# Kernel optimization log

Measured on AMD Instinct MI355X. Metric: run time of the kernel, lower is better.

## Reference

```python
import jax, jax.numpy as jnp
import numpy as np

H = 12          # num_attention_heads
D = 64          # attention_head_size
HID = H * D     # hidden_size = 768
M = 1024        # max_position_embeddings


def setup_inputs() -> dict:
    key = jax.random.key(0)
    ks = jax.random.split(key, 9)
    B, S = 4, 1024
    s = 0.02
    return {
        "hidden_states": jax.random.normal(ks[0], (B, S, HID), jnp.float32),
        "attention_mask": jnp.zeros((B, 1, 1, S), jnp.float32),
        "Wq": jax.random.normal(ks[1], (HID, HID), jnp.float32) * s,
        "bq": jnp.zeros((HID,), jnp.float32),
        "Wk": jax.random.normal(ks[2], (HID, HID), jnp.float32) * s,
        "bk": jnp.zeros((HID,), jnp.float32),
        "Wv": jax.random.normal(ks[3], (HID, HID), jnp.float32) * s,
        "bv": jnp.zeros((HID,), jnp.float32),
        "dist_emb": jax.random.normal(ks[4], (2 * M - 1, D), jnp.float32) * s,
    }


def reference(hidden_states, attention_mask, Wq, bq, Wk, bk, Wv, bv, dist_emb):
    B, S, _ = hidden_states.shape

    def heads(x):  # [B,S,HID] -> [B,H,S,D]
        return x.reshape(B, S, H, D).transpose(0, 2, 1, 3)

    q = heads(hidden_states @ Wq + bq)
    k = heads(hidden_states @ Wk + bk)
    v = heads(hidden_states @ Wv + bv)

    # raw dot-product scores [B,H,S,S]
    scores = jnp.einsum('bhld,bhrd->bhlr', q, k)

    # relative_key_query positional bias
    pos = jnp.arange(S)
    distance = pos[:, None] - pos[None, :] + (M - 1)   # [S,S] in [0, 2M-2]
    pe = dist_emb[distance]                            # [S,S,D]
    scores = scores + jnp.einsum('bhld,lrd->bhlr', q, pe) \
                    + jnp.einsum('bhrd,lrd->bhlr', k, pe)

    scores = scores / jnp.sqrt(jnp.asarray(D, scores.dtype)) + attention_mask
    probs = jax.nn.softmax(scores, axis=-1)            # dropout is identity in eval

    ctx = jnp.einsum('bhlr,bhrd->bhld', probs, v)      # [B,H,S,D]
    ctx = ctx.transpose(0, 2, 1, 3).reshape(B, S, HID)
    return ctx, probs
```

## Files before the change

### kernel.cpp

```cpp
#include <hip/hip_runtime.h>
#include <hip/hip_bf16.h>

#define DEVFN __device__ __forceinline__

typedef __bf16 bf16x8 __attribute__((ext_vector_type(8)));
typedef float f32x4 __attribute__((ext_vector_type(4)));
typedef unsigned short ushort8 __attribute__((ext_vector_type(8)));
typedef unsigned short us4 __attribute__((ext_vector_type(4)));

namespace {

constexpr int S = 1024;
constexpr int HID = 768;
constexpr int NH = 12;
constexpr int HD = 64;

DEVFN unsigned short f2bf(float f) {
  union { float f; unsigned u; } v; v.f = f;
  unsigned r = v.u + 0x7FFF + ((v.u >> 16) & 1);
  return (unsigned short)(r >> 16);
}

DEVFN float bf2f(unsigned short u) {
  union { unsigned u; float f; } v; v.u = ((unsigned)u) << 16; return v.f;
}

DEVFN f32x4 zero4() { return f32x4{0.f, 0.f, 0.f, 0.f}; }

DEVFN f32x4 mfma_bf16(bf16x8 a, bf16x8 b, f32x4 c) {
  return __builtin_amdgcn_mfma_f32_16x16x32_bf16(a, b, c, 0, 0, 0);
}

DEVFN void gload16(void* lds_base, const void* gsrc) {
  __builtin_amdgcn_global_load_lds(
      (const __attribute__((address_space(1))) void*)gsrc,
      (__attribute__((address_space(3))) void*)lds_base, 16, 0, 0);
}

DEVFN bf16x8 frag_ld(const char* tile, int row, int ch) {
  int chs = ch ^ (row & 7);
  return *(const bf16x8*)(tile + row * 128 + chs * 16);
}

__global__ void k0_cvt_x(const float* __restrict__ x, unsigned short* __restrict__ xb) {
  size_t i = (size_t)(blockIdx.x * 256 + threadIdx.x) * 8;
  float4 a = *(const float4*)(x + i);
  float4 c = *(const float4*)(x + i + 4);
  ushort8 o;
  o[0] = f2bf(a.x); o[1] = f2bf(a.y); o[2] = f2bf(a.z); o[3] = f2bf(a.w);
  o[4] = f2bf(c.x); o[5] = f2bf(c.y); o[6] = f2bf(c.z); o[7] = f2bf(c.w);
  *(ushort8*)(xb + i) = o;
}

__global__ void k0_cvt_pe(const float* __restrict__ de, unsigned short* __restrict__ peb) {
  size_t i = (size_t)(blockIdx.x * 256 + threadIdx.x) * 8;
  int row = (int)(i >> 6);
  ushort8 o;
  if (row < 2047) {
    float4 a = *(const float4*)(de + i);
    float4 c = *(const float4*)(de + i + 4);
    o[0] = f2bf(a.x); o[1] = f2bf(a.y); o[2] = f2bf(a.z); o[3] = f2bf(a.w);
    o[4] = f2bf(c.x); o[5] = f2bf(c.y); o[6] = f2bf(c.z); o[7] = f2bf(c.w);
  } else {
    o = ushort8{0, 0, 0, 0, 0, 0, 0, 0};
  }
  *(ushort8*)(peb + i) = o;
}

__global__ __launch_bounds__(256) void k0_wt(const float* __restrict__ Wq,
                                             const float* __restrict__ Wk,
                                             const float* __restrict__ Wv,
                                             unsigned short* __restrict__ wt) {
  __shared__ float t[64][65];
  int bidx = blockIdx.x;
  int sec = bidx / 144, rem = bidx % 144;
  int ktb = rem / 12, ntb = rem % 12;
  const float* W = (sec == 0) ? Wq : ((sec == 1) ? Wk : Wv);
  int k0 = ktb * 64, n0 = ntb * 64;
  int tid = threadIdx.x;
  #pragma unroll
  for (int p = 0; p < 4; ++p) {
    int id = p * 256 + tid;
    int row = id >> 4, ch = id & 15;
    float4 v = *(const float4*)(W + (size_t)(k0 + row) * 768 + n0 + ch * 4);
    t[row][ch * 4 + 0] = v.x; t[row][ch * 4 + 1] = v.y;
    t[row][ch * 4 + 2] = v.z; t[row][ch * 4 + 3] = v.w;
  }
  __syncthreads();
  #pragma unroll
  for (int p = 0; p < 2; ++p) {
    int id = p * 256 + tid;
    int nrow = id >> 3, c8 = id & 7;
    ushort8 o;
    #pragma unroll
    for (int i = 0; i < 8; ++i) o[i] = f2bf(t[c8 * 8 + i][nrow]);
    *(ushort8*)(wt + (size_t)(sec * 768 + n0 + nrow) * 768 + k0 + c8 * 8) = o;
  }
}

__global__ __launch_bounds__(256) void k1_qkv(
    const unsigned short* __restrict__ xb, const unsigned short* __restrict__ wt,
    const float* __restrict__ bq, const float* __restrict__ bk, const float* __restrict__ bv,
    unsigned short* __restrict__ q_ws, unsigned short* __restrict__ k_ws,
    unsigned short* __restrict__ vt_ws) {
  __shared__ char ldsA[8192], ldsB[8192];
  const int tid = threadIdx.x, lane = tid & 63, wv = tid >> 6;
  const int row16 = lane & 15, cgrp = lane >> 4;
  const int ntb = blockIdx.x % 36, mtb = blockIdx.x / 36;
  const int sec = ntb / 12;
  const int n0 = ntb * 64;
  const int m0 = mtb * 64;

  f32x4 acc[4] = {zero4(), zero4(), zero4(), zero4()};

  for (int k0 = 0; k0 < 768; k0 += 64) {
    #pragma unroll
    for (int c = 0; c < 2; ++c) {
      int cc = (wv * 2 + c) * 64 + lane;
      int row = cc >> 3, ch = cc & 7, chs = ch ^ (row & 7);
      gload16(ldsA + (wv * 2 + c) * 1024, xb + (size_t)(m0 + row) * 768 + k0 + chs * 8);
      gload16(ldsB + (wv * 2 + c) * 1024, wt + (size_t)(n0 + row) * 768 + k0 + chs * 8);
    }
    __syncthreads();
    if (sec < 2) {
      bf16x8 af[2];
      #pragma unroll
      for (int k2 = 0; k2 < 2; ++k2) af[k2] = frag_ld(ldsA, wv * 16 + row16, k2 * 4 + cgrp);
      #pragma unroll
      for (int nt = 0; nt < 4; ++nt)
        #pragma unroll
        for (int k2 = 0; k2 < 2; ++k2) {
          bf16x8 bf = frag_ld(ldsB, nt * 16 + row16, k2 * 4 + cgrp);
          acc[nt] = mfma_bf16(af[k2], bf, acc[nt]);
        }
    } else {
      bf16x8 af[2];
      #pragma unroll
      for (int k2 = 0; k2 < 2; ++k2) af[k2] = frag_ld(ldsB, wv * 16 + row16, k2 * 4 + cgrp);
      #pragma unroll
      for (int mt = 0; mt < 4; ++mt)
        #pragma unroll
        for (int k2 = 0; k2 < 2; ++k2) {
          bf16x8 bx = frag_ld(ldsA, mt * 16 + row16, k2 * 4 + cgrp);
          acc[mt] = mfma_bf16(af[k2], bx, acc[mt]);
        }
    }
    __syncthreads();
  }

  if (sec < 2) {
    unsigned short* dst = (sec == 0) ? q_ws : k_ws;
    const float* bias = (sec == 0) ? bq : bk;
    int nl0 = (ntb % 12) * 64;
    #pragma unroll
    for (int nt = 0; nt < 4; ++nt) {
      int nn = nl0 + nt * 16 + row16;
      float bb = bias[nn];
      int hh = nn >> 6, dd = nn & 63;
      #pragma unroll
      for (int j = 0; j < 4; ++j) {
        int m = m0 + wv * 16 + cgrp * 4 + j;
        int b_ = m >> 10, s_ = m & 1023;
        dst[(size_t)((b_ * 12 + hh) * 1024 + s_) * 64 + dd] = f2bf(acc[nt][j] + bb);
      }
    }
  } else {
    int nl0 = (ntb % 12) * 64;
    #pragma unroll
    for (int j = 0; j < 4; ++j) {
      int nn = nl0 + wv * 16 + cgrp * 4 + j;
      float bb = bv[nn];
      int hh = nn >> 6, dd = nn & 63;
      #pragma unroll
      for (int mt = 0; mt < 4; ++mt) {
        int m = m0 + mt * 16 + row16;
        int b_ = m >> 10, s_ = m & 1023;
        vt_ws[(size_t)((b_ * 12 + hh) * 64 + dd) * 1024 + s_] = f2bf(acc[mt][j] + bb);
      }
    }
  }
}

__global__ __launch_bounds__(256) void k2_score(
    const unsigned short* __restrict__ q_ws, const unsigned short* __restrict__ k_ws,
    const unsigned short* __restrict__ peb, const float* __restrict__ mask,
    unsigned short* __restrict__ p_out, float* __restrict__ rsum_part) {
  __shared__ __align__(16) char kpe_lds[24576];
  __shared__ unsigned short p_sh[64 * 64];
  __shared__ float rsum_sh[2][64];

  char* k_lds = kpe_lds;
  char* pe_lds = kpe_lds + 8192;

  const int tid = threadIdx.x, lane = tid & 63, wv = tid >> 6;
  const int wl = wv >> 1, wr = wv & 1;
  const int row16 = lane & 15, cgrp = lane >> 4;

  const int bid = blockIdx.x;
  const int swz = (bid & 7) * 1536 + (bid >> 3);
  const int rt = swz & 15, lt = (swz >> 4) & 15, bh = swz >> 8;
  const int b = bh / NH;
  const int l0 = lt * 64, r0 = rt * 64;

  const unsigned short* qh = q_ws + (size_t)bh * S * HD;
  const unsigned short* khp = k_ws + (size_t)bh * S * HD;
  const float* maskb = mask + b * S;

  #pragma unroll
  for (int c = 0; c < 2; ++c) {
    int cc = (wv * 2 + c) * 64 + lane;
    int row = cc >> 3, ch = cc & 7, chs = ch ^ (row & 7);
    gload16(k_lds + (wv * 2 + c) * 1024, khp + (size_t)(r0 + row) * HD + chs * 8);
  }
  {
    int m0 = l0 - r0 + 960;
    #pragma unroll
    for (int c = 0; c < 4; ++c) {
      int cc = (wv * 4 + c) * 64 + lane;
      int row = cc >> 3, ch = cc & 7, chs = ch ^ (row & 7);
      gload16(pe_lds + (wv * 4 + c) * 1024, peb + (size_t)(m0 + row) * HD + chs * 8);
    }
  }

  bf16x8 qf[2][2];
  #pragma unroll
  for (int ltl = 0; ltl < 2; ++ltl)
    #pragma unroll
    for (int k2 = 0; k2 < 2; ++k2)
      qf[ltl][k2] = *(const bf16x8*)(qh + (size_t)(l0 + wl * 32 + ltl * 16 + row16) * HD +
                                     k2 * 32 + cgrp * 8);
  __syncthreads();

  bf16x8 kf[2][2], pef[4][2];
  #pragma unroll
  for (int rtl = 0; rtl < 2; ++rtl)
    #pragma unroll
    for (int k2 = 0; k2 < 2; ++k2)
      kf[rtl][k2] = frag_ld(k_lds, wr * 32 + rtl * 16 + row16, k2 * 4 + cgrp);
  const int qb = (wl - wr) * 32 + 32;
  #pragma unroll
  for (int jt = 0; jt < 4; ++jt)
    #pragma unroll
    for (int k2 = 0; k2 < 2; ++k2)
      pef[jt][k2] = frag_ld(pe_lds, qb + jt * 16 + row16, k2 * 4 + cgrp);
  __syncthreads();

  unsigned short* s3w = (unsigned short*)kpe_lds + wv * (64 * 36);

  #pragma unroll
  for (int rtl = 0; rtl < 2; ++rtl)
    #pragma unroll
    for (int jt = 0; jt < 4; ++jt) {
      f32x4 a3 = zero4();
      a3 = mfma_bf16(kf[rtl][0], pef[jt][0], a3);
      a3 = mfma_bf16(kf[rtl][1], pef[jt][1], a3);
      us4 o;
      o[0] = f2bf(a3[0]); o[1] = f2bf(a3[1]); o[2] = f2bf(a3[2]); o[3] = f2bf(a3[3]);
      *(us4*)(s3w + (jt * 16 + row16) * 36 + rtl * 16 + cgrp * 4) = o;
    }

  f32x4 s1[2][2];
  #pragma unroll
  for (int ltl = 0; ltl < 2; ++ltl)
    #pragma unroll
    for (int rtl = 0; rtl < 2; ++rtl) {
      f32x4 a1 = zero4();
      a1 = mfma_bf16(qf[ltl][0], kf[rtl][0], a1);
      a1 = mfma_bf16(qf[ltl][1], kf[rtl][1], a1);
      s1[ltl][rtl] = a1;
    }
  f32x4 s2[2][4];
  #pragma unroll
  for (int ltl = 0; ltl < 2; ++ltl)
    #pragma unroll
    for (int jt = 0; jt < 4; ++jt) {
      f32x4 a2 = zero4();
      a2 = mfma_bf16(qf[ltl][0], pef[jt][0], a2);
      a2 = mfma_bf16(qf[ltl][1], pef[jt][1], a2);
      s2[ltl][jt] = a2;
    }

  float rs[2][4] = {};
  #pragma unroll
  for (int rtl = 0; rtl < 2; ++rtl) {
    float mval = maskb[r0 + wr * 32 + rtl * 16 + row16];
    #pragma unroll
    for (int ltl = 0; ltl < 2; ++ltl) {
      const int jtA = ltl - rtl + 1;
      #pragma unroll
      for (int j = 0; j < 4; ++j) {
        int dl = ltl * 16 + cgrp * 4 + j;
        int dr = rtl * 16 + row16;
        int jjq = dl - dr + 31;
        int src = (lane & 48) | (jjq & 15);
        float vA = __shfl(s2[ltl][jtA][j], src, 64);
        float vB = __shfl(s2[ltl][jtA + 1][j], src, 64);
        float b1 = ((jjq >> 4) == jtA) ? vA : vB;
        float b2 = bf2f(s3w[jjq * 36 + dr]);
        float logit = (s1[ltl][rtl][j] + b1 + b2) * 0.125f + mval;
        float p = __expf(logit);
        rs[ltl][j] += p;
        int dlb = wl * 32 + dl, drb = wr * 32 + dr;
        p_sh[dlb * 64 + (drb ^ ((dlb & 7) << 3))] = f2bf(p);
      }
    }
  }

  #pragma unroll
  for (int ltl = 0; ltl < 2; ++ltl)
    #pragma unroll
    for (int j = 0; j < 4; ++j) {
      float v = rs[ltl][j];
      v += __shfl_xor(v, 1, 64);
      v += __shfl_xor(v, 2, 64);
      v += __shfl_xor(v, 4, 64);
      v += __shfl_xor(v, 8, 64);
      rs[ltl][j] = v;
    }
  if (row16 == 0) {
    #pragma unroll
    for (int ltl = 0; ltl < 2; ++ltl)
      #pragma unroll
      for (int j = 0; j < 4; ++j)
        rsum_sh[wr][wl * 32 + ltl * 16 + cgrp * 4 + j] = rs[ltl][j];
  }
  __syncthreads();

  if (tid < 64)
    rsum_part[((size_t)(bh * 16 + lt) * 64 + tid) * 16 + rt] =
        rsum_sh[0][tid] + rsum_sh[1][tid];

  #pragma unroll
  for (int p2 = 0; p2 < 2; ++p2) {
    int id = p2 * 256 + tid, dl = id >> 3, c = id & 7;
    uint4 w = *(const uint4*)((const char*)p_sh + dl * 128 + (c ^ (dl & 7)) * 16);
    *(uint4*)(p_out + ((size_t)bh * S + l0 + dl) * S + r0 + c * 8) = w;
  }
}

__global__ __launch_bounds__(256) void k3_pv(
    const unsigned short* __restrict__ p_in, const unsigned short* __restrict__ vt_ws,
    const float* __restrict__ rsum_part, float* __restrict__ out_ctx,
    float* __restrict__ out_probs) {
  __shared__ char p_sh[2][8192];
  __shared__ float inv_sh[64];

  const int tid = threadIdx.x, lane = tid & 63, wv = tid >> 6;
  const int row16 = lane & 15, cgrp = lane >> 4;
  const int bid = blockIdx.x;
  const int swz = (bid & 7) * 96 + (bid >> 3);
  const int lt = swz & 15, bh = swz >> 4;
  const int b = bh / NH, h = bh % NH;
  const int l0 = lt * 64;

  const unsigned short* vth = vt_ws + (size_t)bh * HD * S;
  float* probs_bh = out_probs + (size_t)bh * S * S;

  if (tid < 64) {
    const float4* pp =
        (const float4*)(rsum_part + ((size_t)(bh * 16 + lt) * 64 + tid) * 16);
    float s = 0.f;
    #pragma unroll
    for (int i = 0; i < 4; ++i) {
      float4 v = pp[i];
      s += v.x + v.y + v.z + v.w;
    }
    inv_sh[tid] = 1.0f / s;
  }

  auto stage = [&](char* buf, int r0) {
    #pragma unroll
    for (int c = 0; c < 2; ++c) {
      int cc = (wv * 2 + c) * 64 + lane;
      int row = cc >> 3, ch = cc & 7, chs = ch ^ (row & 7);
      gload16(buf + (wv * 2 + c) * 1024,
              p_in + ((size_t)bh * S + l0 + row) * S + r0 + chs * 8);
    }
  };

  stage(p_sh[0], 0);
  __syncthreads();

  f32x4 ctxacc[4] = {zero4(), zero4(), zero4(), zero4()};

  for (int rt = 0; rt < 16; ++rt) {
    const int r0 = rt * 64, cur = rt & 1;
    if (rt < 15) stage(p_sh[cur ^ 1], r0 + 64);
    const char* cb = p_sh[cur];

    #pragma unroll
    for (int p2 = 0; p2 < 2; ++p2) {
      int id = p2 * 256 + tid, dl = id >> 3, c = id & 7;
      uint4 w = *(const uint4*)(cb + dl * 128 + (c ^ (dl & 7)) * 16);
      const unsigned short* pu = (const unsigned short*)&w;
      float iv = inv_sh[dl];
      float* dst = probs_bh + (size_t)(l0 + dl) * S + r0 + c * 8;
      float4 lo{bf2f(pu[0]) * iv, bf2f(pu[1]) * iv, bf2f(pu[2]) * iv, bf2f(pu[3]) * iv};
      float4 hi{bf2f(pu[4]) * iv, bf2f(pu[5]) * iv, bf2f(pu[6]) * iv, bf2f(pu[7]) * iv};
      *(float4*)dst = lo; *(float4*)(dst + 4) = hi;
    }

    {
      int lrow = wv * 16 + row16;
      bf16x8 pa[2];
      #pragma unroll
      for (int kc = 0; kc < 2; ++kc) {
        int ch = kc * 4 + cgrp, chs = ch ^ (lrow & 7);
        pa[kc] = *(const bf16x8*)(cb + lrow * 128 + chs * 16);
      }
      #pragma unroll
      for (int dt = 0; dt < 4; ++dt) {
        bf16x8 vb0 = *(const bf16x8*)(vth + (size_t)(dt * 16 + row16) * S + r0 + cgrp * 8);
        bf16x8 vb1 = *(const bf16x8*)(vth + (size_t)(dt * 16 + row16) * S + r0 + 32 + cgrp * 8);
        ctxacc[dt] = mfma_bf16(pa[0], vb0, ctxacc[dt]);
        ctxacc[dt] = mfma_bf16(pa[1], vb1, ctxacc[dt]);
      }
    }
    __syncthreads();
  }

  #pragma unroll
  for (int dt = 0; dt < 4; ++dt)
    #pragma unroll
    for (int j = 0; j < 4; ++j) {
      int lr = wv * 16 + cgrp * 4 + j;
      out_ctx[((size_t)(b * S + l0 + lr)) * HID + h * HD + dt * 16 + row16] =
          ctxacc[dt][j] * inv_sh[lr];
    }
}

}

extern "C" void kernel_launch(void* const* d_in, const int* in_sizes, int n_in,
                              void* d_out, int out_size, void* d_ws, size_t ws_size,
                              hipStream_t stream) {
  const float* hidden = (const float*)d_in[0];
  const float* mask   = (const float*)d_in[1];
  const float* Wq = (const float*)d_in[2];
  const float* bq = (const float*)d_in[3];
  const float* Wk = (const float*)d_in[4];
  const float* bk = (const float*)d_in[5];
  const float* Wv = (const float*)d_in[6];
  const float* bv = (const float*)d_in[7];
  const float* de = (const float*)d_in[8];

  unsigned short* ws = (unsigned short*)d_ws;
  unsigned short* q_ws  = ws;
  unsigned short* k_ws  = ws + 3145728;
  unsigned short* vt_ws = ws + 6291456;
  unsigned short* xb    = ws + 9437184;
  unsigned short* wt    = ws + 12582912;
  unsigned short* peb   = ws + 14352384;
  float* rsum_part = (float*)(ws + 14483456);
  unsigned short* p_ws  = ws + 16056320;

  float* outc = (float*)d_out;
  float* outp = outc + (size_t)4 * 1024 * 768;

  hipLaunchKernelGGL(k0_cvt_x, dim3(1536), dim3(256), 0, stream, hidden, xb);
  hipLaunchKernelGGL(k0_cvt_pe, dim3(64), dim3(256), 0, stream, de, peb);
  hipLaunchKernelGGL(k0_wt, dim3(432), dim3(256), 0, stream, Wq, Wk, Wv, wt);
  hipLaunchKernelGGL(k1_qkv, dim3(2304), dim3(256), 0, stream,
                     xb, wt, bq, bk, bv, q_ws, k_ws, vt_ws);
  hipLaunchKernelGGL(k2_score, dim3(12288), dim3(256), 0, stream,
                     q_ws, k_ws, peb, mask, p_ws, rsum_part);
  hipLaunchKernelGGL(k3_pv, dim3(768), dim3(256), 0, stream,
                     p_ws, vt_ws, rsum_part, outc, outp);
}
```

Baseline: 206.7 us.

## Merge two r-tiles per score block sharing PE staging; fold scale into exp2

The score kernel now runs 512-thread blocks, each covering two adjacent 64-column key tiles. The two halves share one 192-row positional-embedding staging buffer instead of each loading 128 rows, which cuts redundant global loads and halves the number of row-sum partials that the PV kernel must reduce. Separately, the 1/sqrt(D)·log2(e) factor is split as sqrt(0.125·log2e) and pre-multiplied into Q, K and the PE table during their bf16 conversion, so the softmax uses exp2f without a per-element scale. This changes rounding slightly and raises per-block LDS use, which may reduce occupancy.

```diff
diff --git a/kernel.cpp b/kernel.cpp
--- a/kernel.cpp
+++ b/kernel.cpp
@@ -14,6 +14,8 @@
 constexpr int HID = 768;
 constexpr int NH = 12;
 constexpr int HD = 64;
+constexpr float SC = 0.4246609f;
+constexpr float LOG2E = 1.44269504f;
 
 DEVFN unsigned short f2bf(float f) {
   union { float f; unsigned u; } v; v.f = f;
@@ -59,8 +61,8 @@
   if (row < 2047) {
     float4 a = *(const float4*)(de + i);
     float4 c = *(const float4*)(de + i + 4);
-    o[0] = f2bf(a.x); o[1] = f2bf(a.y); o[2] = f2bf(a.z); o[3] = f2bf(a.w);
-    o[4] = f2bf(c.x); o[5] = f2bf(c.y); o[6] = f2bf(c.z); o[7] = f2bf(c.w);
+    o[0] = f2bf(a.x * SC); o[1] = f2bf(a.y * SC); o[2] = f2bf(a.z * SC); o[3] = f2bf(a.w * SC);
+    o[4] = f2bf(c.x * SC); o[5] = f2bf(c.y * SC); o[6] = f2bf(c.z * SC); o[7] = f2bf(c.w * SC);
   } else {
     o = ushort8{0, 0, 0, 0, 0, 0, 0, 0};
   }
@@ -161,7 +163,7 @@
       for (int j = 0; j < 4; ++j) {
         int m = m0 + wv * 16 + cgrp * 4 + j;
         int b_ = m >> 10, s_ = m & 1023;
-        dst[(size_t)((b_ * 12 + hh) * 1024 + s_) * 64 + dd] = f2bf(acc[nt][j] + bb);
+        dst[(size_t)((b_ * 12 + hh) * 1024 + s_) * 64 + dd] = f2bf((acc[nt][j] + bb) * SC);
       }
     }
   } else {
@@ -181,30 +183,36 @@
   }
 }
 
-__global__ __launch_bounds__(256) void k2_score(
+__global__ __launch_bounds__(512) void k2_score(
     const unsigned short* __restrict__ q_ws, const unsigned short* __restrict__ k_ws,
     const unsigned short* __restrict__ peb, const float* __restrict__ mask,
     unsigned short* __restrict__ p_out, float* __restrict__ rsum_part) {
-  __shared__ __align__(16) char kpe_lds[24576];
-  __shared__ unsigned short p_sh[64 * 64];
-  __shared__ float rsum_sh[2][64];
-
-  char* k_lds = kpe_lds;
-  char* pe_lds = kpe_lds + 8192;
-
-  const int tid = threadIdx.x, lane = tid & 63, wv = tid >> 6;
+  __shared__ __align__(16) char stage_lds[40960];
+  __shared__ unsigned short p_sh[2][64 * 64];
+  __shared__ float rsum_sh[4][64];
+
+  const int tid = threadIdx.x, lane = tid & 63;
+  const int wv8 = tid >> 6;
+  const int quad = wv8 >> 2;
+  const int wv = wv8 & 3;
   const int wl = wv >> 1, wr = wv & 1;
   const int row16 = lane & 15, cgrp = lane >> 4;
 
   const int bid = blockIdx.x;
-  const int swz = (bid & 7) * 1536 + (bid >> 3);
-  const int rt = swz & 15, lt = (swz >> 4) & 15, bh = swz >> 8;
+  const int swz = (bid & 7) * 768 + (bid >> 3);
+  const int rq = swz & 7, lt = (swz >> 3) & 15, bh = swz >> 7;
   const int b = bh / NH;
-  const int l0 = lt * 64, r0 = rt * 64;
+  const int l0 = lt * 64;
+  const int rt = rq * 2 + quad;
+  const int r0 = rt * 64;
 
   const unsigned short* qh = q_ws + (size_t)bh * S * HD;
   const unsigned short* khp = k_ws + (size_t)bh * S * HD;
   const float* maskb = mask + b * S;
+
+  char* k_lds = stage_lds + quad * 8192;
+  char* pe_lds = stage_lds + 16384;
+  const int peoff = 64 * (1 - quad);
 
   #pragma unroll
   for (int c = 0; c < 2; ++c) {
@@ -213,12 +221,12 @@
     gload16(k_lds + (wv * 2 + c) * 1024, khp + (size_t)(r0 + row) * HD + chs * 8);
   }
   {
-    int m0 = l0 - r0 + 960;
-    #pragma unroll
-    for (int c = 0; c < 4; ++c) {
-      int cc = (wv * 4 + c) * 64 + lane;
+    int mU = l0 - rq * 128 - 64 + 960;
+    #pragma unroll
+    for (int c = 0; c < 3; ++c) {
+      int cc = (wv8 * 3 + c) * 64 + lane;
       int row = cc >> 3, ch = cc & 7, chs = ch ^ (row & 7);
-      gload16(pe_lds + (wv * 4 + c) * 1024, peb + (size_t)(m0 + row) * HD + chs * 8);
+      gload16(pe_lds + (wv8 * 3 + c) * 1024, peb + (size_t)(mU + row) * HD + chs * 8);
     }
   }
 
@@ -237,7 +245,7 @@
     #pragma unroll
     for (int k2 = 0; k2 < 2; ++k2)
       kf[rtl][k2] = frag_ld(k_lds, wr * 32 + rtl * 16 + row16, k2 * 4 + cgrp);
-  const int qb = (wl - wr) * 32 + 32;
+  const int qb = (wl - wr) * 32 + 32 + peoff;
   #pragma unroll
   for (int jt = 0; jt < 4; ++jt)
     #pragma unroll
@@ -245,7 +253,7 @@
       pef[jt][k2] = frag_ld(pe_lds, qb + jt * 16 + row16, k2 * 4 + cgrp);
   __syncthreads();
 
-  unsigned short* s3w = (unsigned short*)kpe_lds + wv * (64 * 36);
+  unsigned short* s3w = (unsigned short*)stage_lds + wv8 * (64 * 36);
 
   #pragma unroll
   for (int rtl = 0; rtl < 2; ++rtl)
@@ -283,7 +291,7 @@
   float rs[2][4] = {};
   #pragma unroll
   for (int rtl = 0; rtl < 2; ++rtl) {
-    float mval = maskb[r0 + wr * 32 + rtl * 16 + row16];
+    float mval = maskb[r0 + wr * 32 + rtl * 16 + row16] * LOG2E;
     #pragma unroll
     for (int ltl = 0; ltl < 2; ++ltl) {
       const int jtA = ltl - rtl + 1;
@@ -297,11 +305,10 @@
         float vB = __shfl(s2[ltl][jtA + 1][j], src, 64);
         float b1 = ((jjq >> 4) == jtA) ? vA : vB;
         float b2 = bf2f(s3w[jjq * 36 + dr]);
-        float logit = (s1[ltl][rtl][j] + b1 + b2) * 0.125f + mval;
-        float p = __expf(logit);
+        float p = exp2f(s1[ltl][rtl][j] + b1 + b2 + mval);
         rs[ltl][j] += p;
         int dlb = wl * 32 + dl, drb = wr * 32 + dr;
-        p_sh[dlb * 64 + (drb ^ ((dlb & 7) << 3))] = f2bf(p);
+        p_sh[quad][dlb * 64 + (drb ^ ((dlb & 7) << 3))] = f2bf(p);
       }
     }
   }
@@ -322,19 +329,22 @@
     for (int ltl = 0; ltl < 2; ++ltl)
       #pragma unroll
       for (int j = 0; j < 4; ++j)
-        rsum_sh[wr][wl * 32 + ltl * 16 + cgrp * 4 + j] = rs[ltl][j];
+        rsum_sh[quad * 2 + wr][wl * 32 + ltl * 16 + cgrp * 4 + j] = rs[ltl][j];
   }
   __syncthreads();
 
   if (tid < 64)
-    rsum_part[((size_t)(bh * 16 + lt) * 64 + tid) * 16 + rt] =
-        rsum_sh[0][tid] + rsum_sh[1][tid];
-
-  #pragma unroll
-  for (int p2 = 0; p2 < 2; ++p2) {
-    int id = p2 * 256 + tid, dl = id >> 3, c = id & 7;
-    uint4 w = *(const uint4*)((const char*)p_sh + dl * 128 + (c ^ (dl & 7)) * 16);
-    *(uint4*)(p_out + ((size_t)bh * S + l0 + dl) * S + r0 + c * 8) = w;
+    rsum_part[((size_t)(bh * 16 + lt) * 64 + tid) * 8 + rq] =
+        rsum_sh[0][tid] + rsum_sh[1][tid] + rsum_sh[2][tid] + rsum_sh[3][tid];
+
+  {
+    const int t256 = tid & 255;
+    #pragma unroll
+    for (int p2 = 0; p2 < 2; ++p2) {
+      int id = p2 * 256 + t256, dl = id >> 3, c = id & 7;
+      uint4 w = *(const uint4*)((const char*)p_sh[quad] + dl * 128 + (c ^ (dl & 7)) * 16);
+      *(uint4*)(p_out + ((size_t)bh * S + l0 + dl) * S + r0 + c * 8) = w;
+    }
   }
 }
 
@@ -358,14 +368,9 @@
 
   if (tid < 64) {
     const float4* pp =
-        (const float4*)(rsum_part + ((size_t)(bh * 16 + lt) * 64 + tid) * 16);
-    float s = 0.f;
-    #pragma unroll
-    for (int i = 0; i < 4; ++i) {
-      float4 v = pp[i];
-      s += v.x + v.y + v.z + v.w;
-    }
-    inv_sh[tid] = 1.0f / s;
+        (const float4*)(rsum_part + ((size_t)(bh * 16 + lt) * 64 + tid) * 8);
+    float4 v0 = pp[0], v1 = pp[1];
+    inv_sh[tid] = 1.0f / (v0.x + v0.y + v0.z + v0.w + v1.x + v1.y + v1.z + v1.w);
   }
 
   auto stage = [&](char* buf, int r0) {
@@ -462,7 +467,7 @@
   hipLaunchKernelGGL(k0_wt, dim3(432), dim3(256), 0, stream, Wq, Wk, Wv, wt);
   hipLaunchKernelGGL(k1_qkv, dim3(2304), dim3(256), 0, stream,
                      xb, wt, bq, bk, bv, q_ws, k_ws, vt_ws);
-  hipLaunchKernelGGL(k2_score, dim3(12288), dim3(256), 0, stream,
+  hipLaunchKernelGGL(k2_score, dim3(6144), dim3(512), 0, stream,
                      q_ws, k_ws, peb, mask, p_ws, rsum_part);
   hipLaunchKernelGGL(k3_pv, dim3(768), dim3(256), 0, stream,
                      p_ws, vt_ws, rsum_part, outc, outp);
```

Measured after the change: 200.3 us. 3.1% less time.
